# Kernel optimization log

Hardware: AMD Instinct MI355X
Metric: run time of the kernel (lower is better)

Reference implementation:

```python
import jax, jax.numpy as jnp
import numpy as np
from jax import lax

# Dims
HID = 2048          # hidden_size
DI = 4096           # d_inner = expand * hidden
NH = 64             # mamba heads
P = 64              # head dim
N = 128             # d_state
G = 1               # n_groups
K = 4               # conv kernel
IM = 8192           # MLP intermediate
BB, L = 2, 2048
EPS = 1e-5
CONV_DIM = DI + 2 * G * N            # 4352
D_IN_PROJ = 2 * DI + 2 * G * N + NH  # 8512


def rmsnorm(x, w, eps=EPS):
    v = jnp.mean(jnp.square(x), axis=-1, keepdims=True)
    return x * jax.lax.rsqrt(v + eps) * w


def setup_inputs() -> dict:
    key = jax.random.key(0)
    ks = jax.random.split(key, 16)
    s = 0.02
    return {
        "positions": jnp.broadcast_to(jnp.arange(L, dtype=jnp.int32), (BB, L)),
        "hidden_states": jax.random.normal(ks[0], (BB, L, HID), jnp.float32),
        "residual": jax.random.normal(ks[1], (BB, L, HID), jnp.float32),
        "in_proj_w": jax.random.normal(ks[2], (D_IN_PROJ, HID), jnp.float32) * s,
        "conv_w": jax.random.normal(ks[3], (CONV_DIM, K), jnp.float32) * 0.2,
        "conv_b": jax.random.normal(ks[4], (CONV_DIM,), jnp.float32) * 0.02,
        "A_log": jnp.log(jnp.arange(1, NH + 1, dtype=jnp.float32)),
        "D": jnp.ones((NH,), jnp.float32),
        "dt_bias": jax.random.uniform(ks[5], (NH,), jnp.float32, -4.0, -2.0),
        "mixer_norm_w": jnp.ones((DI,), jnp.float32),
        "out_proj_w": jax.random.normal(ks[6], (HID, DI), jnp.float32) * s,
        "input_ln_w": jnp.ones((HID,), jnp.float32),
        "pre_ff_ln_w": jnp.ones((HID,), jnp.float32),
        "gate_up_w": jax.random.normal(ks[7], (2 * IM, HID), jnp.float32) * s,
        "down_w": jax.random.normal(ks[8], (HID, IM), jnp.float32) * s,
    }


def reference(positions, hidden_states, residual, in_proj_w, conv_w, conv_b,
              A_log, D, dt_bias, mixer_norm_w, out_proj_w, input_ln_w,
              pre_ff_ln_w, gate_up_w, down_w):
    del positions  # not used by the mamba mixer math
    B_, Lq, _ = hidden_states.shape

    # --- input RMSNorm with fused residual add ---
    residual = hidden_states + residual
    hs = rmsnorm(residual, input_ln_w)

    # --- Mamba2 mixer ---
    proj = jnp.einsum('bld,ed->ble', hs, in_proj_w)   # [B,L,D_IN_PROJ]
    z = proj[..., :DI]
    xBC = proj[..., DI:DI + CONV_DIM]
    dt = proj[..., DI + CONV_DIM:]                    # [B,L,NH]

    # causal depthwise conv (kernel K) + SiLU
    xp = jnp.pad(xBC, ((0, 0), (K - 1, 0), (0, 0)))
    conv = conv_b
    for k in range(K):
        conv = conv + xp[:, k:k + Lq, :] * conv_w[:, k]
    xBC = jax.nn.silu(conv)

    x = xBC[..., :DI].reshape(B_, Lq, NH, P)
    Bm = xBC[..., DI:DI + G * N].reshape(B_, Lq, G, N)
    Cm = xBC[..., DI + G * N:].reshape(B_, Lq, G, N)
    rep = NH // G
    Bm = jnp.repeat(Bm, rep, axis=2)                  # [B,L,NH,N]
    Cm = jnp.repeat(Cm, rep, axis=2)

    dt = jax.nn.softplus(dt + dt_bias)                # [B,L,NH]
    A = -jnp.exp(A_log)                               # [NH]
    dA = jnp.exp(dt * A)                              # [B,L,NH]

    def step(h, inp):
        x_t, B_t, C_t, dA_t, dt_t = inp               # [B,NH,P],[B,NH,N],[B,NH,N],[B,NH],[B,NH]
        h = dA_t[..., None, None] * h + \
            (dt_t[..., None, None] * x_t[..., None]) * B_t[:, :, None, :]
        y = jnp.einsum('bhpn,bhn->bhp', h, C_t)
        return h, y

    xs = (x.transpose(1, 0, 2, 3), Bm.transpose(1, 0, 2, 3),
          Cm.transpose(1, 0, 2, 3), dA.transpose(1, 0, 2), dt.transpose(1, 0, 2))
    h0 = jnp.zeros((B_, NH, P, N), hidden_states.dtype)
    _, ys = lax.scan(step, h0, xs)                    # [L,B,NH,P]
    y = ys.transpose(1, 0, 2, 3) + D[None, None, :, None] * x
    y = y.reshape(B_, Lq, DI)

    # gated RMSNorm (Mixer2RMSNormGated, n_groups=1)
    y = y * jax.nn.silu(z)
    y = rmsnorm(y, mixer_norm_w)
    mamba_out = jnp.einsum('bld,hd->blh', y, out_proj_w)

    # --- pre-FF RMSNorm with fused residual add ---
    residual2 = mamba_out + residual
    hs2 = rmsnorm(residual2, pre_ff_ln_w)

    # --- gated MLP (SiluAndMul) ---
    gu = jnp.einsum('bld,ed->ble', hs2, gate_up_w)    # [B,L,2*IM]
    act = jax.nn.silu(gu[..., :IM]) * gu[..., IM:]
    out = jnp.einsum('bli,hi->blh', act, down_w)
    return out, residual2
```

## Files before the change

### kernel.cpp

```cpp
#include <hip/hip_runtime.h>

#define T_TOK 4096
#define HID   2048
#define DI    4096
#define NH    64
#define PDIM  64
#define NSTATE 128
#define IM    8192
#define LSEQ  2048
#define CONVD 4352
#define DPROJ 8512
#define DPADR 8704
#define QC    64
#define NCH   32

typedef __bf16 bf16x8 __attribute__((ext_vector_type(8)));
typedef float  f32x4  __attribute__((ext_vector_type(4)));

__device__ __forceinline__ unsigned short f2bf(float f) {
  unsigned u = __float_as_uint(f);
  u = (u + 0x7fffu + ((u >> 16) & 1u)) >> 16;
  return (unsigned short)u;
}
__device__ __forceinline__ float bf2f(unsigned short h) {
  return __uint_as_float(((unsigned)h) << 16);
}
__device__ __forceinline__ float siluf(float x) {
  return x / (1.f + __expf(-x));
}

#define GLL(gaddr, laddr) __builtin_amdgcn_global_load_lds( \
    (const __attribute__((address_space(1))) void*)(gaddr), \
    (__attribute__((address_space(3))) void*)(laddr), 16, 0, 0)

__device__ __forceinline__ void cvt8(const float* __restrict__ s, unsigned short* __restrict__ d) {
  float4 v0 = *(const float4*)s;
  float4 v1 = *(const float4*)(s + 4);
  unsigned short o[8];
  o[0] = f2bf(v0.x); o[1] = f2bf(v0.y); o[2] = f2bf(v0.z); o[3] = f2bf(v0.w);
  o[4] = f2bf(v1.x); o[5] = f2bf(v1.y); o[6] = f2bf(v1.z); o[7] = f2bf(v1.w);
  *(uint4*)d = *(const uint4*)o;
}

#define CV_IN_END  2228224ULL
#define CV_OUT_END 3276800ULL
#define CV_GU_END  7471104ULL
#define CV_DN_END  9568256ULL

__global__ __launch_bounds__(256)
void k_cvt_all(const float* __restrict__ w_in, const float* __restrict__ w_out,
               const float* __restrict__ w_gu, const float* __restrict__ w_dn,
               unsigned short* __restrict__ d_in, unsigned short* __restrict__ d_out,
               unsigned short* __restrict__ d_gu, unsigned short* __restrict__ d_dn) {
  size_t gid = (size_t)blockIdx.x * 256 + threadIdx.x;
  if (gid < CV_IN_END) {
    size_t idx8 = gid * 8;
    int r = (int)(idx8 >> 11), k = (int)(idx8 & 2047);
    if (r < DPROJ) {
      cvt8(&w_in[(size_t)r * HID + k], d_in + idx8);
    } else {
      uint4 z = {0, 0, 0, 0};
      *(uint4*)(d_in + idx8) = z;
    }
  } else if (gid < CV_OUT_END) {
    size_t idx8 = (gid - CV_IN_END) * 8;
    cvt8(w_out + idx8, d_out + idx8);
  } else if (gid < CV_GU_END) {
    size_t idx8 = (gid - CV_OUT_END) * 8;
    int r = (int)(idx8 >> 11), k = (int)(idx8 & 2047);
    int g = r >> 6, j = r & 63;
    int srcr = (j < 32) ? (g * 32 + j) : (IM + g * 32 + (j - 32));
    cvt8(&w_gu[(size_t)srcr * HID + k], d_gu + idx8);
  } else if (gid < CV_DN_END) {
    size_t idx8 = (gid - CV_GU_END) * 8;
    cvt8(w_dn + idx8, d_dn + idx8);
  }
}

template <int EPI, int BM>
__global__ __launch_bounds__(512, 2)
void gemm8(const unsigned short* __restrict__ A, const unsigned short* __restrict__ W,
           int K, int ldo, void* __restrict__ outp,
           const float* __restrict__ resid) {
  constexpr int MREP  = BM / 32;
  constexpr int ABYT  = BM * 128;
  constexpr int BUFB  = ABYT + 32768;
  constexpr int NTM   = 4096 / BM;
  __shared__ __align__(16) char smem[2 * BUFB];
  const int t = threadIdx.x;
  const int w = t >> 6, l = t & 63;
  const int lr = l & 15, hi = l >> 4;
  const int wr = w >> 2, wc = w & 3;

  const int q = (int)gridDim.x >> 3;
  const int bid = blockIdx.x;
  const int id2 = (bid & 7) * q + (bid >> 3);
  const int tn = id2 / NTM, tm = id2 % NTM;
  const int m0b = tm * BM, n0b = tn << 8;

  const int srow = t >> 3;
  const int scole = ((t & 7) << 3) ^ ((t & 32) ? 16 : 0) ^ ((t & 64) ? 32 : 0);
  const unsigned short* Ag = A + (size_t)(m0b + srow) * K + scole;
  const unsigned short* Wg = W + (size_t)(n0b + srow) * K + scole;
  const int ldsw = w * 1024;

  const int fa = ((lr & 4) ? 32 : 0) | ((lr & 8) ? 64 : 0);
  const int arow = (wr * (BM / 2) + lr) * 128 + hi * 16;
  const int brow = (wc * 64 + lr) * 128 + hi * 16;
  const int aoff0 = arow ^ fa, aoff1 = (arow + 64) ^ fa;
  const int boff0 = brow ^ fa, boff1 = (brow + 64) ^ fa;

#define ISSUE_A(jt, bb) do {                                                    \
    _Pragma("unroll")                                                           \
    for (int p_ = 0; p_ < BM / 64; ++p_)                                        \
      GLL(Ag + (size_t)(p_ * 64) * K + (size_t)(jt) * 64,                       \
          smem + (bb) * BUFB + p_ * 8192 + ldsw); } while (0)
#define ISSUE_B(jt, bb) do {                                                    \
    _Pragma("unroll")                                                           \
    for (int p_ = 0; p_ < 4; ++p_)                                              \
      GLL(Wg + (size_t)(p_ * 64) * K + (size_t)(jt) * 64,                       \
          smem + (bb) * BUFB + ABYT + p_ * 8192 + ldsw); } while (0)

#define RDF(off, base) (*(const bf16x8*)((base) + (off)))
#define MF(P, x, y, c0, c1, c2, c3) do {                                                     \
    __builtin_amdgcn_s_setprio(1);                                                           \
    acc[2*(P)  ][0] = __builtin_amdgcn_mfma_f32_16x16x32_bf16((x),(c0),acc[2*(P)  ][0],0,0,0);\
    acc[2*(P)+1][0] = __builtin_amdgcn_mfma_f32_16x16x32_bf16((y),(c0),acc[2*(P)+1][0],0,0,0);\
    acc[2*(P)  ][1] = __builtin_amdgcn_mfma_f32_16x16x32_bf16((x),(c1),acc[2*(P)  ][1],0,0,0);\
    acc[2*(P)+1][1] = __builtin_amdgcn_mfma_f32_16x16x32_bf16((y),(c1),acc[2*(P)+1][1],0,0,0);\
    acc[2*(P)  ][2] = __builtin_amdgcn_mfma_f32_16x16x32_bf16((x),(c2),acc[2*(P)  ][2],0,0,0);\
    acc[2*(P)+1][2] = __builtin_amdgcn_mfma_f32_16x16x32_bf16((y),(c2),acc[2*(P)+1][2],0,0,0);\
    acc[2*(P)  ][3] = __builtin_amdgcn_mfma_f32_16x16x32_bf16((x),(c3),acc[2*(P)  ][3],0,0,0);\
    acc[2*(P)+1][3] = __builtin_amdgcn_mfma_f32_16x16x32_bf16((y),(c3),acc[2*(P)+1][3],0,0,0);\
    __builtin_amdgcn_s_setprio(0); } while (0)

  f32x4 acc[MREP][4];
#pragma unroll
  for (int m = 0; m < MREP; m++)
#pragma unroll
    for (int n = 0; n < 4; n++) acc[m][n] = (f32x4){0.f, 0.f, 0.f, 0.f};

  const int nkt = K >> 6;
  ISSUE_A(0, 0); ISSUE_B(0, 0);

  for (int j = 0; j < nkt; ++j) {
    const int cur = j & 1;
    const char* Ab = smem + cur * BUFB;
    const char* Bb = Ab + ABYT;
    asm volatile("s_waitcnt vmcnt(0)" ::: "memory");
    __builtin_amdgcn_s_barrier();
    __builtin_amdgcn_sched_barrier(0);
    if (j + 1 < nkt) { ISSUE_A(j + 1, cur ^ 1); ISSUE_B(j + 1, cur ^ 1); }
    bf16x8 b0 = RDF(boff0, Bb), b1 = RDF(boff0 + 2048, Bb),
           b2 = RDF(boff0 + 4096, Bb), b3 = RDF(boff0 + 6144, Bb);
    bf16x8 af0 = RDF(aoff0, Ab), af1 = RDF(aoff0 + 2048, Ab);
    bf16x8 af2, af3, b4, b5, b6, b7;
    if constexpr (MREP == 8) {
      af2 = RDF(aoff0 + 4096, Ab); af3 = RDF(aoff0 + 6144, Ab);
      MF(0, af0, af1, b0, b1, b2, b3);
      af0 = RDF(aoff0 + 8192, Ab); af1 = RDF(aoff0 + 10240, Ab);
      MF(1, af2, af3, b0, b1, b2, b3);
      af2 = RDF(aoff0 + 12288, Ab); af3 = RDF(aoff0 + 14336, Ab);
      MF(2, af0, af1, b0, b1, b2, b3);
      b4 = RDF(boff1, Bb); b5 = RDF(boff1 + 2048, Bb);
      b6 = RDF(boff1 + 4096, Bb); b7 = RDF(boff1 + 6144, Bb);
      af0 = RDF(aoff1, Ab); af1 = RDF(aoff1 + 2048, Ab);
      MF(3, af2, af3, b0, b1, b2, b3);
      af2 = RDF(aoff1 + 4096, Ab); af3 = RDF(aoff1 + 6144, Ab);
      MF(0, af0, af1, b4, b5, b6, b7);
      af0 = RDF(aoff1 + 8192, Ab); af1 = RDF(aoff1 + 10240, Ab);
      MF(1, af2, af3, b4, b5, b6, b7);
      af2 = RDF(aoff1 + 12288, Ab); af3 = RDF(aoff1 + 14336, Ab);
      MF(2, af0, af1, b4, b5, b6, b7);
      MF(3, af2, af3, b4, b5, b6, b7);
    } else {
      af2 = RDF(aoff0 + 4096, Ab); af3 = RDF(aoff0 + 6144, Ab);
      MF(0, af0, af1, b0, b1, b2, b3);
      b4 = RDF(boff1, Bb); b5 = RDF(boff1 + 2048, Bb);
      b6 = RDF(boff1 + 4096, Bb); b7 = RDF(boff1 + 6144, Bb);
      af0 = RDF(aoff1, Ab); af1 = RDF(aoff1 + 2048, Ab);
      MF(1, af2, af3, b0, b1, b2, b3);
      af2 = RDF(aoff1 + 4096, Ab); af3 = RDF(aoff1 + 6144, Ab);
      MF(0, af0, af1, b4, b5, b6, b7);
      MF(1, af2, af3, b4, b5, b6, b7);
    }
  }

  if constexpr (EPI == 0) {
    unsigned short* op = (unsigned short*)outp;
#pragma unroll
    for (int m = 0; m < MREP; m++)
#pragma unroll
      for (int n = 0; n < 4; n++)
#pragma unroll
        for (int r = 0; r < 4; r++) {
          int row = m0b + wr * (BM / 2) + m * 16 + hi * 4 + r;
          int col = n0b + wc * 64 + n * 16 + lr;
          op[(size_t)row * ldo + col] = f2bf(acc[m][n][r]);
        }
  } else if constexpr (EPI == 2) {
    unsigned short* op = (unsigned short*)outp;
    const int gbase = (n0b + wc * 64) >> 1;
#pragma unroll
    for (int m = 0; m < MREP; m++)
#pragma unroll
      for (int n = 0; n < 2; n++)
#pragma unroll
        for (int r = 0; r < 4; r++) {
          int row = m0b + wr * (BM / 2) + m * 16 + hi * 4 + r;
          int col = gbase + n * 16 + lr;
          float g = acc[m][n][r], u = acc[m][n + 2][r];
          op[(size_t)row * ldo + col] = f2bf(siluf(g) * u);
        }
  } else {
    float* op = (float*)outp;
#pragma unroll
    for (int m = 0; m < MREP; m++)
#pragma unroll
      for (int n = 0; n < 4; n++)
#pragma unroll
        for (int r = 0; r < 4; r++) {
          int row = m0b + wr * (BM / 2) + m * 16 + hi * 4 + r;
          int col = n0b + wc * 64 + n * 16 + lr;
          float v = acc[m][n][r];
          if constexpr (EPI == 1) v += resid[(size_t)row * ldo + col];
          op[(size_t)row * ldo + col] = v;
        }
  }
#undef ISSUE_A
#undef ISSUE_B
#undef RDF
#undef MF
}

__device__ __forceinline__ float block_reduce_sum256(float v, float* sred) {
#pragma unroll
  for (int m = 32; m; m >>= 1) v += __shfl_xor(v, m);
  int t = threadIdx.x;
  if ((t & 63) == 0) sred[t >> 6] = v;
  __syncthreads();
  return sred[0] + sred[1] + sred[2] + sred[3];
}

__global__ __launch_bounds__(256)
void k_addnorm(const float* __restrict__ hin, const float* __restrict__ rin,
               const float* __restrict__ wln, float* __restrict__ rout,
               unsigned short* __restrict__ hbf) {
  __shared__ float sred[4];
  const int tok = blockIdx.x, t = threadIdx.x;
  const size_t base = (size_t)tok * HID + t * 8;
  float4 a0 = *(const float4*)&hin[base];
  float4 a1 = *(const float4*)&hin[base + 4];
  float4 b0 = *(const float4*)&rin[base];
  float4 b1 = *(const float4*)&rin[base + 4];
  float v[8] = {a0.x + b0.x, a0.y + b0.y, a0.z + b0.z, a0.w + b0.w,
                a1.x + b1.x, a1.y + b1.y, a1.z + b1.z, a1.w + b1.w};
  float ss = 0.f;
#pragma unroll
  for (int j = 0; j < 8; j++) ss += v[j] * v[j];
  float tot = block_reduce_sum256(ss, sred);
  float rms = rsqrtf(tot * (1.f / HID) + 1e-5f);
  *(float4*)&rout[base] = (float4){v[0], v[1], v[2], v[3]};
  *(float4*)&rout[base + 4] = (float4){v[4], v[5], v[6], v[7]};
  float4 w0 = *(const float4*)&wln[t * 8];
  float4 w1 = *(const float4*)&wln[t * 8 + 4];
  float wa[8] = {w0.x, w0.y, w0.z, w0.w, w1.x, w1.y, w1.z, w1.w};
  unsigned short o[8];
#pragma unroll
  for (int j = 0; j < 8; j++) o[j] = f2bf(v[j] * rms * wa[j]);
  *(ushort4*)&hbf[base] = *(ushort4*)&o[0];
  *(ushort4*)&hbf[base + 4] = *(ushort4*)&o[4];
}

__global__ __launch_bounds__(256)
void k_rmsnorm_bf(const float* __restrict__ src, const float* __restrict__ wln,
                  unsigned short* __restrict__ dst) {
  __shared__ float sred[4];
  const int tok = blockIdx.x, t = threadIdx.x;
  const size_t base = (size_t)tok * HID + t * 8;
  float4 a0 = *(const float4*)&src[base];
  float4 a1 = *(const float4*)&src[base + 4];
  float v[8] = {a0.x, a0.y, a0.z, a0.w, a1.x, a1.y, a1.z, a1.w};
  float ss = 0.f;
#pragma unroll
  for (int j = 0; j < 8; j++) ss += v[j] * v[j];
  float tot = block_reduce_sum256(ss, sred);
  float rms = rsqrtf(tot * (1.f / HID) + 1e-5f);
  float4 w0 = *(const float4*)&wln[t * 8];
  float4 w1 = *(const float4*)&wln[t * 8 + 4];
  float wa[8] = {w0.x, w0.y, w0.z, w0.w, w1.x, w1.y, w1.z, w1.w};
  unsigned short o[8];
#pragma unroll
  for (int j = 0; j < 8; j++) o[j] = f2bf(v[j] * rms * wa[j]);
  *(ushort4*)&dst[base] = *(ushort4*)&o[0];
  *(ushort4*)&dst[base + 4] = *(ushort4*)&o[4];
}

__global__ __launch_bounds__(256)
void k_gatenorm(const unsigned short* __restrict__ ybuf, const unsigned short* __restrict__ projbf,
                const float* __restrict__ wmix, unsigned short* __restrict__ ynorm) {
  __shared__ float sred[4];
  const int tok = blockIdx.x, t = threadIdx.x;
  const size_t yb = (size_t)tok * DI;
  const size_t pb = (size_t)tok * DPADR;
  float g[16];
  float ss = 0.f;
#pragma unroll
  for (int j = 0; j < 16; j++) {
    int idx = j * 256 + t;
    float yv = bf2f(ybuf[yb + idx]);
    float z = bf2f(projbf[pb + idx]);
    float gg = yv * siluf(z);
    g[j] = gg;
    ss += gg * gg;
  }
  float tot = block_reduce_sum256(ss, sred);
  float rms = rsqrtf(tot * (1.f / DI) + 1e-5f);
#pragma unroll
  for (int j = 0; j < 16; j++) {
    int idx = j * 256 + t;
    ynorm[yb + idx] = f2bf(g[j] * rms * wmix[idx]);
  }
}

__global__ __launch_bounds__(256)
void k_conv(const unsigned short* __restrict__ projbf, const float* __restrict__ cw,
            const float* __restrict__ cb, const float* __restrict__ dt_bias,
            unsigned short* __restrict__ xbf, unsigned short* __restrict__ bcbf,
            float* __restrict__ dtg) {
  const int c = blockIdx.x * 256 + threadIdx.x;
  const int tk = blockIdx.y;
  if (c < CONVD) {
    const int lpos = tk & (LSEQ - 1);
    float4 wv = *(const float4*)&cw[c * 4];
    float wk[4] = {wv.x, wv.y, wv.z, wv.w};
    float acc = cb[c];
#pragma unroll
    for (int k = 0; k < 4; k++) {
      int lp = lpos - 3 + k;
      if (lp >= 0) acc += bf2f(projbf[(size_t)(tk - 3 + k) * DPADR + DI + c]) * wk[k];
    }
    unsigned short r = f2bf(siluf(acc));
    if (c < DI) xbf[(size_t)tk * DI + c] = r;
    else        bcbf[(size_t)tk * 256 + (c - DI)] = r;
  } else if (c < CONVD + NH) {
    const int hh = c - CONVD;
    float x = bf2f(projbf[(size_t)tk * DPADR + DI + c]) + dt_bias[hh];
    float dt = (x > 20.f) ? x : log1pf(__expf(x));
    dtg[(size_t)tk * NH + hh] = dt;
  }
}

__global__ __launch_bounds__(256)
void k_ssd1(const unsigned short* __restrict__ xbf, const unsigned short* __restrict__ bcbf,
            const float* __restrict__ dtg, const float* __restrict__ A_log,
            const float* __restrict__ Dv, unsigned short* __restrict__ ybuf,
            unsigned short* __restrict__ Sc, float* __restrict__ dtsum) {
  __shared__ __align__(16) char smem[60928];
  unsigned short* sBs  = (unsigned short*)(smem);
  unsigned short* sCs  = (unsigned short*)(smem + 16384);
  unsigned short* sMs  = (unsigned short*)(smem + 16384);
  unsigned short* sBsT = (unsigned short*)(smem + 32768);
  unsigned short* sXsT = (unsigned short*)(smem + 51200);
  float* sdt = (float*)(smem + 60416);
  float* sdl = (float*)(smem + 60672);

  const int bi = blockIdx.x;
  const int ch = bi & 31, h = (bi >> 5) & 63, b = bi >> 11;
  const int bh = b * NH + h;
  const int tok0 = b * LSEQ + ch * QC;
  const int t = threadIdx.x;
  const int w = t >> 6, l = t & 63, lr = l & 15, hi = l >> 4;
  const float Ah = -__expf(A_log[h]);
  const float Dh = Dv[h];

  {
    const int srow = t >> 4, scol = (t & 15) * 8;
#pragma unroll
    for (int i = 0; i < 4; i++) {
      const unsigned short* gb = bcbf + (size_t)(tok0 + srow + 16 * i) * 256 + scol;
      GLL(gb, (char*)sBs + i * 4096 + w * 1024);
      GLL(gb + 128, (char*)sCs + i * 4096 + w * 1024);
    }
  }
  if (t < QC) sdt[t] = dtg[(size_t)(tok0 + t) * NH + h];
  __syncthreads();
  if (t < QC) sdl[t] = sdt[t];
  __syncthreads();
  for (int off = 1; off < QC; off <<= 1) {
    float v = 0.f;
    if (t < QC && t >= off) v = sdl[t - off];
    __syncthreads();
    if (t < QC) sdl[t] += v;
    __syncthreads();
  }

  {
    const int s = t >> 2;
    const float DlQ = sdl[QC - 1];
    const float csc = __expf(Ah * (DlQ - sdl[s])) * sdt[s];
    const int n0 = (t & 3) * 32;
#pragma unroll
    for (int j = 0; j < 32; j++) {
      float bv = bf2f(sBs[s * 128 + n0 + j]);
      sBsT[(n0 + j) * 72 + s] = f2bf(csc * bv);
    }
    const int p0 = (t & 3) * 16;
    const unsigned short* gx = xbf + (size_t)(tok0 + s) * DI + h * 64 + p0;
    union { uint4 v; unsigned short u[8]; } x0, x1;
    x0.v = *(const uint4*)gx;
    x1.v = *(const uint4*)(gx + 8);
#pragma unroll
    for (int j = 0; j < 8; j++) {
      sXsT[(p0 + j) * 72 + s] = x0.u[j];
      sXsT[(p0 + 8 + j) * 72 + s] = x1.u[j];
    }
  }
  __syncthreads();

  f32x4 accS[4];
#pragma unroll
  for (int jf = 0; jf < 4; jf++) accS[jf] = (f32x4){0.f, 0.f, 0.f, 0.f};
#pragma unroll
  for (int ks = 0; ks < 4; ks++) {
    bf16x8 a = *(const bf16x8*)&sBs[(w * 16 + lr) * 128 + ks * 32 + hi * 8];
#pragma unroll
    for (int jf = 0; jf < 4; jf++) {
      bf16x8 bbq = *(const bf16x8*)&sCs[(jf * 16 + lr) * 128 + ks * 32 + hi * 8];
      accS[jf] = __builtin_amdgcn_mfma_f32_16x16x32_bf16(a, bbq, accS[jf], 0, 0, 0);
    }
  }
  __syncthreads();

  {
    const int s0 = w * 16 + hi * 4;
#pragma unroll
    for (int jf = 0; jf < 4; jf++) {
      const int tt = jf * 16 + lr;
      const float dlt = sdl[tt];
      unsigned short mv[4];
#pragma unroll
      for (int r = 0; r < 4; r++) {
        const int ss = s0 + r;
        float val = 0.f;
        if (ss <= tt) val = accS[jf][r] * __expf(Ah * (dlt - sdl[ss])) * sdt[ss];
        mv[r] = f2bf(val);
      }
      *(ushort4*)&sMs[tt * 72 + s0] = *(ushort4*)mv;
    }
  }
  __syncthreads();

  {
    f32x4 accY[4];
#pragma unroll
    for (int jf = 0; jf < 4; jf++) accY[jf] = (f32x4){0.f, 0.f, 0.f, 0.f};
#pragma unroll
    for (int ks = 0; ks < 2; ks++) {
      bf16x8 a = *(const bf16x8*)&sMs[(w * 16 + lr) * 72 + ks * 32 + hi * 8];
#pragma unroll
      for (int jf = 0; jf < 4; jf++) {
        bf16x8 bbq = *(const bf16x8*)&sXsT[(jf * 16 + lr) * 72 + ks * 32 + hi * 8];
        accY[jf] = __builtin_amdgcn_mfma_f32_16x16x32_bf16(a, bbq, accY[jf], 0, 0, 0);
      }
    }
#pragma unroll
    for (int jf = 0; jf < 4; jf++)
#pragma unroll
      for (int r = 0; r < 4; r++) {
        const int tt = w * 16 + hi * 4 + r;
        const int pp = jf * 16 + lr;
        float xv = bf2f(sXsT[pp * 72 + tt]);
        ybuf[(size_t)(tok0 + tt) * DI + h * 64 + pp] = f2bf(accY[jf][r] + Dh * xv);
      }
  }

  {
    f32x4 accT[8];
#pragma unroll
    for (int jf = 0; jf < 8; jf++) accT[jf] = (f32x4){0.f, 0.f, 0.f, 0.f};
#pragma unroll
    for (int ks = 0; ks < 2; ks++) {
      bf16x8 a = *(const bf16x8*)&sXsT[(w * 16 + lr) * 72 + ks * 32 + hi * 8];
#pragma unroll
      for (int jf = 0; jf < 8; jf++) {
        bf16x8 bbq = *(const bf16x8*)&sBsT[(jf * 16 + lr) * 72 + ks * 32 + hi * 8];
        accT[jf] = __builtin_amdgcn_mfma_f32_16x16x32_bf16(a, bbq, accT[jf], 0, 0, 0);
      }
    }
    unsigned short* sc = Sc + ((size_t)bh * NCH + ch) * (PDIM * NSTATE);
#pragma unroll
    for (int jf = 0; jf < 8; jf++)
#pragma unroll
      for (int r = 0; r < 4; r++) {
        const int pp = w * 16 + hi * 4 + r;
        const int nn = jf * 16 + lr;
        sc[pp * NSTATE + nn] = f2bf(accT[jf][r]);
      }
  }
  if (t == 0) dtsum[bh * NCH + ch] = sdl[QC - 1];
}

__global__ __launch_bounds__(256)
void k_ssd2(const float* __restrict__ A_log, const float* __restrict__ dtsum,
            unsigned short* __restrict__ ScHt) {
  const int blk = blockIdx.x;
  const int bh = blk >> 3, pg = blk & 7;
  const int t = threadIdx.x;
  const int p = pg * 8 + (t >> 5), n0 = (t & 31) * 4;
  const int h = bh & 63;
  const float Ah = -__expf(A_log[h]);
  float H[4] = {0.f, 0.f, 0.f, 0.f};
  for (int c = 0; c < NCH; c++) {
    size_t base = (((size_t)bh * NCH + c) * PDIM + p) * NSTATE + n0;
    ushort4 sv = *(const ushort4*)&ScHt[base];
    float dec = __expf(Ah * dtsum[bh * NCH + c]);
    ushort4 hv;
    hv.x = f2bf(H[0]); hv.y = f2bf(H[1]); hv.z = f2bf(H[2]); hv.w = f2bf(H[3]);
    *(ushort4*)&ScHt[base] = hv;
    H[0] = dec * H[0] + bf2f(sv.x);
    H[1] = dec * H[1] + bf2f(sv.y);
    H[2] = dec * H[2] + bf2f(sv.z);
    H[3] = dec * H[3] + bf2f(sv.w);
  }
}

__global__ __launch_bounds__(256)
void k_ssd3(const unsigned short* __restrict__ bcbf, const unsigned short* __restrict__ Ht,
            const float* __restrict__ dtg, const float* __restrict__ A_log,
            unsigned short* __restrict__ ybuf) {
  __shared__ __align__(16) char smem[33280];
  unsigned short* sCs = (unsigned short*)(smem);
  unsigned short* sHt = (unsigned short*)(smem + 16384);
  float* sdt = (float*)(smem + 32768);
  float* sdl = (float*)(smem + 33024);

  const int bi = blockIdx.x;
  const int ch = bi & 31, h = (bi >> 5) & 63, b = bi >> 11;
  const int bh = b * NH + h;
  const int tok0 = b * LSEQ + ch * QC;
  const int t = threadIdx.x;
  const int w = t >> 6, l = t & 63, lr = l & 15, hi = l >> 4;
  const float Ah = -__expf(A_log[h]);

  {
    const int srow = t >> 4, scol = (t & 15) * 8;
    const unsigned short* gh = Ht + ((size_t)bh * NCH + ch) * (PDIM * NSTATE);
#pragma unroll
    for (int i = 0; i < 4; i++) {
      const unsigned short* gc = bcbf + (size_t)(tok0 + srow + 16 * i) * 256 + 128 + scol;
      GLL(gc, (char*)sCs + i * 4096 + w * 1024);
      GLL(gh + i * 2048 + t * 8, (char*)sHt + i * 4096 + w * 1024);
    }
  }
  if (t < QC) sdt[t] = dtg[(size_t)(tok0 + t) * NH + h];
  __syncthreads();
  if (t < QC) sdl[t] = sdt[t];
  __syncthreads();
  for (int off = 1; off < QC; off <<= 1) {
    float v = 0.f;
    if (t < QC && t >= off) v = sdl[t - off];
    __syncthreads();
    if (t < QC) sdl[t] += v;
    __syncthreads();
  }

  f32x4 acc[4];
#pragma unroll
  for (int jf = 0; jf < 4; jf++) acc[jf] = (f32x4){0.f, 0.f, 0.f, 0.f};
#pragma unroll
  for (int ks = 0; ks < 4; ks++) {
    bf16x8 a = *(const bf16x8*)&sCs[(w * 16 + lr) * 128 + ks * 32 + hi * 8];
#pragma unroll
    for (int jf = 0; jf < 4; jf++) {
      bf16x8 bbq = *(const bf16x8*)&sHt[(jf * 16 + lr) * 128 + ks * 32 + hi * 8];
      acc[jf] = __builtin_amdgcn_mfma_f32_16x16x32_bf16(a, bbq, acc[jf], 0, 0, 0);
    }
  }
#pragma unroll
  for (int jf = 0; jf < 4; jf++)
#pragma unroll
    for (int r = 0; r < 4; r++) {
      const int tt = w * 16 + hi * 4 + r;
      const int pp = jf * 16 + lr;
      const float dec = __expf(Ah * sdl[tt]);
      const size_t o = (size_t)(tok0 + tt) * DI + h * 64 + pp;
      ybuf[o] = f2bf(bf2f(ybuf[o]) + dec * acc[jf][r]);
    }
}

static const size_t OFF_WBF_IN  = 0;
static const size_t OFF_WBF_OUT = 35651584;
static const size_t OFF_WBF_GU  = 52428800;
static const size_t OFF_WBF_DN  = 119537664;
static const size_t OFF_RESID   = 153092096;
static const size_t OFF_HSBF    = 186646528;
static const size_t OFF_PROJ    = 203423744;
static const size_t OFF_XBF     = 274726912;
static const size_t OFF_BCBF    = 308281344;
static const size_t OFF_DTG     = 310378496;
static const size_t OFF_YBUF    = 311427072;
static const size_t OFF_SC      = 344981504;
static const size_t OFF_DTSUM   = 412090368;

extern "C" void kernel_launch(void* const* d_in, const int* in_sizes, int n_in,
                              void* d_out, int out_size, void* d_ws, size_t ws_size,
                              hipStream_t stream) {
  (void)in_sizes; (void)n_in; (void)out_size; (void)ws_size;
  const float* hidden   = (const float*)d_in[1];
  const float* resin    = (const float*)d_in[2];
  const float* w_inproj = (const float*)d_in[3];
  const float* conv_w   = (const float*)d_in[4];
  const float* conv_b   = (const float*)d_in[5];
  const float* A_log    = (const float*)d_in[6];
  const float* Dvec     = (const float*)d_in[7];
  const float* dt_bias  = (const float*)d_in[8];
  const float* w_mix    = (const float*)d_in[9];
  const float* w_outp   = (const float*)d_in[10];
  const float* w_ln1    = (const float*)d_in[11];
  const float* w_ln2    = (const float*)d_in[12];
  const float* w_gu     = (const float*)d_in[13];
  const float* w_dn     = (const float*)d_in[14];

  char* ws = (char*)d_ws;
  unsigned short* wbf_in  = (unsigned short*)(ws + OFF_WBF_IN);
  unsigned short* wbf_out = (unsigned short*)(ws + OFF_WBF_OUT);
  unsigned short* wbf_gu  = (unsigned short*)(ws + OFF_WBF_GU);
  unsigned short* wbf_dn  = (unsigned short*)(ws + OFF_WBF_DN);
  float*          residb  = (float*)(ws + OFF_RESID);
  unsigned short* hsbf    = (unsigned short*)(ws + OFF_HSBF);
  unsigned short* projbf  = (unsigned short*)(ws + OFF_PROJ);
  unsigned short* actbf   = (unsigned short*)(ws + OFF_PROJ);
  unsigned short* xbf     = (unsigned short*)(ws + OFF_XBF);
  unsigned short* ynormbf = (unsigned short*)(ws + OFF_XBF);
  unsigned short* bcbf    = (unsigned short*)(ws + OFF_BCBF);
  float*          dtgb    = (float*)(ws + OFF_DTG);
  unsigned short* ybuf    = (unsigned short*)(ws + OFF_YBUF);
  unsigned short* scht    = (unsigned short*)(ws + OFF_SC);
  float*          dtsumb  = (float*)(ws + OFF_DTSUM);

  float* out0 = (float*)d_out;
  float* res2 = out0 + (size_t)T_TOK * HID;

  k_cvt_all<<<37376, 256, 0, stream>>>(w_inproj, w_outp, w_gu, w_dn,
                                       wbf_in, wbf_out, wbf_gu, wbf_dn);
  k_addnorm<<<T_TOK, 256, 0, stream>>>(hidden, resin, w_ln1, residb, hsbf);
  gemm8<0, 256><<<34 * 16, 512, 0, stream>>>(hsbf, wbf_in, HID, DPADR, projbf, nullptr);
  k_conv<<<dim3(18, T_TOK), 256, 0, stream>>>(projbf, conv_w, conv_b, dt_bias, xbf, bcbf, dtgb);
  k_ssd1<<<4096, 256, 0, stream>>>(xbf, bcbf, dtgb, A_log, Dvec, ybuf, scht, dtsumb);
  k_ssd2<<<1024, 256, 0, stream>>>(A_log, dtsumb, scht);
  k_ssd3<<<4096, 256, 0, stream>>>(bcbf, scht, dtgb, A_log, ybuf);
  k_gatenorm<<<T_TOK, 256, 0, stream>>>(ybuf, projbf, w_mix, ynormbf);
  gemm8<1, 128><<<8 * 32, 512, 0, stream>>>(ynormbf, wbf_out, DI, HID, res2, residb);
  k_rmsnorm_bf<<<T_TOK, 256, 0, stream>>>(res2, w_ln2, hsbf);
  gemm8<2, 256><<<64 * 16, 512, 0, stream>>>(hsbf, wbf_gu, HID, IM, actbf, nullptr);
  gemm8<3, 128><<<8 * 32, 512, 0, stream>>>(actbf, wbf_dn, IM, HID, out0, nullptr);
}
```

Baseline: 996.4 us.

## Replace GEMM with fixed 128x256 tile, K-step 32, unswizzled LDS, 4 blocks/CU

Replaces the templated BM GEMM with a single kernel that uses a 128x256 output tile, a K step of 32 and an unswizzled 64-byte-row LDS layout. Shared memory per block drops to 48KB and the launch bound asks for 4 blocks per CU to raise occupancy. All four projection GEMMs use it, so the in_proj and gate_up GEMMs now run smaller M tiles with twice as many blocks. The cost is fewer MFMAs per barrier, more barrier round-trips, and likely LDS bank conflicts because the XOR swizzle is gone.

```diff
diff --git a/kernel.cpp b/kernel.cpp
--- a/kernel.cpp
+++ b/kernel.cpp
@@ -77,124 +77,85 @@
   }
 }
 
-template <int EPI, int BM>
-__global__ __launch_bounds__(512, 2)
-void gemm8(const unsigned short* __restrict__ A, const unsigned short* __restrict__ W,
+template <int EPI>
+__global__ __launch_bounds__(512, 4)
+void gemmk(const unsigned short* __restrict__ A, const unsigned short* __restrict__ W,
            int K, int ldo, void* __restrict__ outp,
            const float* __restrict__ resid) {
-  constexpr int MREP  = BM / 32;
-  constexpr int ABYT  = BM * 128;
-  constexpr int BUFB  = ABYT + 32768;
-  constexpr int NTM   = 4096 / BM;
+  constexpr int ABYT = 8192;
+  constexpr int BBYT = 16384;
+  constexpr int BUFB = ABYT + BBYT;
+  constexpr int NTM  = 32;
   __shared__ __align__(16) char smem[2 * BUFB];
   const int t = threadIdx.x;
   const int w = t >> 6, l = t & 63;
   const int lr = l & 15, hi = l >> 4;
   const int wr = w >> 2, wc = w & 3;
 
-  const int q = (int)gridDim.x >> 3;
+  const int q8 = (int)gridDim.x >> 3;
   const int bid = blockIdx.x;
-  const int id2 = (bid & 7) * q + (bid >> 3);
+  const int id2 = (bid & 7) * q8 + (bid >> 3);
   const int tn = id2 / NTM, tm = id2 % NTM;
-  const int m0b = tm * BM, n0b = tn << 8;
-
-  const int srow = t >> 3;
-  const int scole = ((t & 7) << 3) ^ ((t & 32) ? 16 : 0) ^ ((t & 64) ? 32 : 0);
-  const unsigned short* Ag = A + (size_t)(m0b + srow) * K + scole;
-  const unsigned short* Wg = W + (size_t)(n0b + srow) * K + scole;
-  const int ldsw = w * 1024;
-
-  const int fa = ((lr & 4) ? 32 : 0) | ((lr & 8) ? 64 : 0);
-  const int arow = (wr * (BM / 2) + lr) * 128 + hi * 16;
-  const int brow = (wc * 64 + lr) * 128 + hi * 16;
-  const int aoff0 = arow ^ fa, aoff1 = (arow + 64) ^ fa;
-  const int boff0 = brow ^ fa, boff1 = (brow + 64) ^ fa;
-
-#define ISSUE_A(jt, bb) do {                                                    \
-    _Pragma("unroll")                                                           \
-    for (int p_ = 0; p_ < BM / 64; ++p_)                                        \
-      GLL(Ag + (size_t)(p_ * 64) * K + (size_t)(jt) * 64,                       \
-          smem + (bb) * BUFB + p_ * 8192 + ldsw); } while (0)
+  const int m0b = tm << 7, n0b = tn << 8;
+
+  const unsigned short* Ag = A + (size_t)(m0b + (t >> 2)) * K + (t & 3) * 8;
+  const unsigned short* Wg = W + (size_t)(n0b + (t >> 2)) * K + (t & 3) * 8;
+
+  const int aoffc = (wr * 64 + lr) * 64 + hi * 16;
+  const int boffc = ABYT + (wc * 64 + lr) * 64 + hi * 16;
+
+#define ISSUE_A(jt, bb) GLL(Ag + (size_t)(jt) * 32, smem + (bb) * BUFB + t * 16)
 #define ISSUE_B(jt, bb) do {                                                    \
-    _Pragma("unroll")                                                           \
-    for (int p_ = 0; p_ < 4; ++p_)                                              \
-      GLL(Wg + (size_t)(p_ * 64) * K + (size_t)(jt) * 64,                       \
-          smem + (bb) * BUFB + ABYT + p_ * 8192 + ldsw); } while (0)
+    GLL(Wg + (size_t)(jt) * 32, smem + (bb) * BUFB + ABYT + t * 16);            \
+    GLL(Wg + (size_t)128 * K + (size_t)(jt) * 32,                               \
+        smem + (bb) * BUFB + ABYT + 8192 + t * 16); } while (0)
 
 #define RDF(off, base) (*(const bf16x8*)((base) + (off)))
-#define MF(P, x, y, c0, c1, c2, c3) do {                                                     \
-    __builtin_amdgcn_s_setprio(1);                                                           \
-    acc[2*(P)  ][0] = __builtin_amdgcn_mfma_f32_16x16x32_bf16((x),(c0),acc[2*(P)  ][0],0,0,0);\
-    acc[2*(P)+1][0] = __builtin_amdgcn_mfma_f32_16x16x32_bf16((y),(c0),acc[2*(P)+1][0],0,0,0);\
-    acc[2*(P)  ][1] = __builtin_amdgcn_mfma_f32_16x16x32_bf16((x),(c1),acc[2*(P)  ][1],0,0,0);\
-    acc[2*(P)+1][1] = __builtin_amdgcn_mfma_f32_16x16x32_bf16((y),(c1),acc[2*(P)+1][1],0,0,0);\
-    acc[2*(P)  ][2] = __builtin_amdgcn_mfma_f32_16x16x32_bf16((x),(c2),acc[2*(P)  ][2],0,0,0);\
-    acc[2*(P)+1][2] = __builtin_amdgcn_mfma_f32_16x16x32_bf16((y),(c2),acc[2*(P)+1][2],0,0,0);\
-    acc[2*(P)  ][3] = __builtin_amdgcn_mfma_f32_16x16x32_bf16((x),(c3),acc[2*(P)  ][3],0,0,0);\
-    acc[2*(P)+1][3] = __builtin_amdgcn_mfma_f32_16x16x32_bf16((y),(c3),acc[2*(P)+1][3],0,0,0);\
+#define MF2(P, x, y) do {                                                                     \
+    __builtin_amdgcn_s_setprio(1);                                                            \
+    acc[2*(P)  ][0] = __builtin_amdgcn_mfma_f32_16x16x32_bf16((x), b0, acc[2*(P)  ][0],0,0,0);\
+    acc[2*(P)+1][0] = __builtin_amdgcn_mfma_f32_16x16x32_bf16((y), b0, acc[2*(P)+1][0],0,0,0);\
+    acc[2*(P)  ][1] = __builtin_amdgcn_mfma_f32_16x16x32_bf16((x), b1, acc[2*(P)  ][1],0,0,0);\
+    acc[2*(P)+1][1] = __builtin_amdgcn_mfma_f32_16x16x32_bf16((y), b1, acc[2*(P)+1][1],0,0,0);\
+    acc[2*(P)  ][2] = __builtin_amdgcn_mfma_f32_16x16x32_bf16((x), b2, acc[2*(P)  ][2],0,0,0);\
+    acc[2*(P)+1][2] = __builtin_amdgcn_mfma_f32_16x16x32_bf16((y), b2, acc[2*(P)+1][2],0,0,0);\
+    acc[2*(P)  ][3] = __builtin_amdgcn_mfma_f32_16x16x32_bf16((x), b3, acc[2*(P)  ][3],0,0,0);\
+    acc[2*(P)+1][3] = __builtin_amdgcn_mfma_f32_16x16x32_bf16((y), b3, acc[2*(P)+1][3],0,0,0);\
     __builtin_amdgcn_s_setprio(0); } while (0)
 
-  f32x4 acc[MREP][4];
-#pragma unroll
-  for (int m = 0; m < MREP; m++)
+  f32x4 acc[4][4];
+#pragma unroll
+  for (int m = 0; m < 4; m++)
 #pragma unroll
     for (int n = 0; n < 4; n++) acc[m][n] = (f32x4){0.f, 0.f, 0.f, 0.f};
 
-  const int nkt = K >> 6;
+  const int nkt = K >> 5;
   ISSUE_A(0, 0); ISSUE_B(0, 0);
 
   for (int j = 0; j < nkt; ++j) {
-    const int cur = j & 1;
-    const char* Ab = smem + cur * BUFB;
-    const char* Bb = Ab + ABYT;
+    const char* Ab = smem + (size_t)(j & 1) * BUFB;
+    const int nb = (j & 1) ^ 1;
     asm volatile("s_waitcnt vmcnt(0)" ::: "memory");
     __builtin_amdgcn_s_barrier();
     __builtin_amdgcn_sched_barrier(0);
-    if (j + 1 < nkt) { ISSUE_A(j + 1, cur ^ 1); ISSUE_B(j + 1, cur ^ 1); }
-    bf16x8 b0 = RDF(boff0, Bb), b1 = RDF(boff0 + 2048, Bb),
-           b2 = RDF(boff0 + 4096, Bb), b3 = RDF(boff0 + 6144, Bb);
-    bf16x8 af0 = RDF(aoff0, Ab), af1 = RDF(aoff0 + 2048, Ab);
-    bf16x8 af2, af3, b4, b5, b6, b7;
-    if constexpr (MREP == 8) {
-      af2 = RDF(aoff0 + 4096, Ab); af3 = RDF(aoff0 + 6144, Ab);
-      MF(0, af0, af1, b0, b1, b2, b3);
-      af0 = RDF(aoff0 + 8192, Ab); af1 = RDF(aoff0 + 10240, Ab);
-      MF(1, af2, af3, b0, b1, b2, b3);
-      af2 = RDF(aoff0 + 12288, Ab); af3 = RDF(aoff0 + 14336, Ab);
-      MF(2, af0, af1, b0, b1, b2, b3);
-      b4 = RDF(boff1, Bb); b5 = RDF(boff1 + 2048, Bb);
-      b6 = RDF(boff1 + 4096, Bb); b7 = RDF(boff1 + 6144, Bb);
-      af0 = RDF(aoff1, Ab); af1 = RDF(aoff1 + 2048, Ab);
-      MF(3, af2, af3, b0, b1, b2, b3);
-      af2 = RDF(aoff1 + 4096, Ab); af3 = RDF(aoff1 + 6144, Ab);
-      MF(0, af0, af1, b4, b5, b6, b7);
-      af0 = RDF(aoff1 + 8192, Ab); af1 = RDF(aoff1 + 10240, Ab);
-      MF(1, af2, af3, b4, b5, b6, b7);
-      af2 = RDF(aoff1 + 12288, Ab); af3 = RDF(aoff1 + 14336, Ab);
-      MF(2, af0, af1, b4, b5, b6, b7);
-      MF(3, af2, af3, b4, b5, b6, b7);
-    } else {
-      af2 = RDF(aoff0 + 4096, Ab); af3 = RDF(aoff0 + 6144, Ab);
-      MF(0, af0, af1, b0, b1, b2, b3);
-      b4 = RDF(boff1, Bb); b5 = RDF(boff1 + 2048, Bb);
-      b6 = RDF(boff1 + 4096, Bb); b7 = RDF(boff1 + 6144, Bb);
-      af0 = RDF(aoff1, Ab); af1 = RDF(aoff1 + 2048, Ab);
-      MF(1, af2, af3, b0, b1, b2, b3);
-      af2 = RDF(aoff1 + 4096, Ab); af3 = RDF(aoff1 + 6144, Ab);
-      MF(0, af0, af1, b4, b5, b6, b7);
-      MF(1, af2, af3, b4, b5, b6, b7);
-    }
+    if (j + 1 < nkt) { ISSUE_A(j + 1, nb); ISSUE_B(j + 1, nb); }
+    bf16x8 b0 = RDF(boffc, Ab), b1 = RDF(boffc + 1024, Ab),
+           b2 = RDF(boffc + 2048, Ab), b3 = RDF(boffc + 3072, Ab);
+    bf16x8 a0 = RDF(aoffc, Ab), a1 = RDF(aoffc + 1024, Ab);
+    MF2(0, a0, a1);
+    bf16x8 a2 = RDF(aoffc + 2048, Ab), a3 = RDF(aoffc + 3072, Ab);
+    MF2(1, a2, a3);
   }
 
   if constexpr (EPI == 0) {
     unsigned short* op = (unsigned short*)outp;
 #pragma unroll
-    for (int m = 0; m < MREP; m++)
+    for (int m = 0; m < 4; m++)
 #pragma unroll
       for (int n = 0; n < 4; n++)
 #pragma unroll
         for (int r = 0; r < 4; r++) {
-          int row = m0b + wr * (BM / 2) + m * 16 + hi * 4 + r;
+          int row = m0b + wr * 64 + m * 16 + hi * 4 + r;
           int col = n0b + wc * 64 + n * 16 + lr;
           op[(size_t)row * ldo + col] = f2bf(acc[m][n][r]);
         }
@@ -202,12 +163,12 @@
     unsigned short* op = (unsigned short*)outp;
     const int gbase = (n0b + wc * 64) >> 1;
 #pragma unroll
-    for (int m = 0; m < MREP; m++)
+    for (int m = 0; m < 4; m++)
 #pragma unroll
       for (int n = 0; n < 2; n++)
 #pragma unroll
         for (int r = 0; r < 4; r++) {
-          int row = m0b + wr * (BM / 2) + m * 16 + hi * 4 + r;
+          int row = m0b + wr * 64 + m * 16 + hi * 4 + r;
           int col = gbase + n * 16 + lr;
           float g = acc[m][n][r], u = acc[m][n + 2][r];
           op[(size_t)row * ldo + col] = f2bf(siluf(g) * u);
@@ -215,12 +176,12 @@
   } else {
     float* op = (float*)outp;
 #pragma unroll
-    for (int m = 0; m < MREP; m++)
+    for (int m = 0; m < 4; m++)
 #pragma unroll
       for (int n = 0; n < 4; n++)
 #pragma unroll
         for (int r = 0; r < 4; r++) {
-          int row = m0b + wr * (BM / 2) + m * 16 + hi * 4 + r;
+          int row = m0b + wr * 64 + m * 16 + hi * 4 + r;
           int col = n0b + wc * 64 + n * 16 + lr;
           float v = acc[m][n][r];
           if constexpr (EPI == 1) v += resid[(size_t)row * ldo + col];
@@ -230,7 +191,7 @@
 #undef ISSUE_A
 #undef ISSUE_B
 #undef RDF
-#undef MF
+#undef MF2
 }
 
 __device__ __forceinline__ float block_reduce_sum256(float v, float* sred) {
@@ -645,14 +606,14 @@
   k_cvt_all<<<37376, 256, 0, stream>>>(w_inproj, w_outp, w_gu, w_dn,
                                        wbf_in, wbf_out, wbf_gu, wbf_dn);
   k_addnorm<<<T_TOK, 256, 0, stream>>>(hidden, resin, w_ln1, residb, hsbf);
-  gemm8<0, 256><<<34 * 16, 512, 0, stream>>>(hsbf, wbf_in, HID, DPADR, projbf, nullptr);
+  gemmk<0><<<34 * 32, 512, 0, stream>>>(hsbf, wbf_in, HID, DPADR, projbf, nullptr);
   k_conv<<<dim3(18, T_TOK), 256, 0, stream>>>(projbf, conv_w, conv_b, dt_bias, xbf, bcbf, dtgb);
   k_ssd1<<<4096, 256, 0, stream>>>(xbf, bcbf, dtgb, A_log, Dvec, ybuf, scht, dtsumb);
   k_ssd2<<<1024, 256, 0, stream>>>(A_log, dtsumb, scht);
   k_ssd3<<<4096, 256, 0, stream>>>(bcbf, scht, dtgb, A_log, ybuf);
   k_gatenorm<<<T_TOK, 256, 0, stream>>>(ybuf, projbf, w_mix, ynormbf);
-  gemm8<1, 128><<<8 * 32, 512, 0, stream>>>(ynormbf, wbf_out, DI, HID, res2, residb);
+  gemmk<1><<<8 * 32, 512, 0, stream>>>(ynormbf, wbf_out, DI, HID, res2, residb);
   k_rmsnorm_bf<<<T_TOK, 256, 0, stream>>>(res2, w_ln2, hsbf);
-  gemm8<2, 256><<<64 * 16, 512, 0, stream>>>(hsbf, wbf_gu, HID, IM, actbf, nullptr);
-  gemm8<3, 128><<<8 * 32, 512, 0, stream>>>(actbf, wbf_dn, IM, HID, out0, nullptr);
-}
+  gemmk<2><<<64 * 32, 512, 0, stream>>>(hsbf, wbf_gu, HID, IM, actbf, nullptr);
+  gemmk<3><<<8 * 32, 512, 0, stream>>>(actbf, wbf_dn, IM, HID, out0, nullptr);
+}
```

New measurement: 1.123 ms. 1.13x slower.

## Add ping-pong pipelined 256x256 GEMM kernel for in_proj and gate_up

Applied to the files above, without the earlier changes.

Introduces gemm8p, a 256x256-tile GEMM with one block per CU that splits each K-tile's global-to-LDS staging into quarter chunks interleaved with the MFMA phases. It uses per-quarter barriers, s_setprio around the MFMA bursts and partial vmcnt waits so loads overlap compute better than the old double-buffered loop. The in_proj and gate_up GEMMs now use it, and the old gemm8 is trimmed to the BM=128 path. The trade-off is 128KB of LDS per block and occupancy of one block per CU, plus more barriers per tile.

```diff
diff --git a/kernel.cpp b/kernel.cpp
--- a/kernel.cpp
+++ b/kernel.cpp
@@ -77,6 +77,153 @@
   }
 }
 
+template <int EPI>
+__global__ __launch_bounds__(512, 1)
+void gemm8p(const unsigned short* __restrict__ A, const unsigned short* __restrict__ W,
+            int K, int ldo, void* __restrict__ outp) {
+  __shared__ __align__(16) char smem[131072];
+  const int t = threadIdx.x;
+  const int w = t >> 6, l = t & 63;
+  const int lr = l & 15, hi = l >> 4;
+  const int wr = w >> 2, wc = w & 3;
+
+  const int q8 = (int)gridDim.x >> 3;
+  const int bid = blockIdx.x;
+  const int id2 = (bid & 7) * q8 + (bid >> 3);
+  const int tn = id2 >> 4, tm = id2 & 15;
+  const int m0b = tm << 8, n0b = tn << 8;
+
+  const int srow = t >> 3;
+  const int scole = ((t & 7) << 3) ^ ((t & 32) ? 16 : 0) ^ ((t & 64) ? 32 : 0);
+  const unsigned short* Ag = A + (size_t)(m0b + srow) * K + scole;
+  const unsigned short* Wg = W + (size_t)(n0b + srow) * K + scole;
+  const int ldsw = w * 1024;
+
+  const int fa = ((lr & 4) ? 32 : 0) | ((lr & 8) ? 64 : 0);
+  const int arow = (wr * 128 + lr) * 128 + hi * 16;
+  const int brow = (wc * 64 + lr) * 128 + hi * 16;
+  const int aoff0 = arow ^ fa, aoff1 = (arow + 64) ^ fa;
+  const int boff0 = brow ^ fa, boff1 = (brow + 64) ^ fa;
+
+#define STAGE_A(jt, h, bb) do {                                                 \
+    _Pragma("unroll")                                                           \
+    for (int p_ = 0; p_ < 2; ++p_)                                              \
+      GLL(Ag + (size_t)((h) * 128 + p_ * 64) * K + (size_t)(jt) * 64,           \
+          smem + (bb) * 65536 + ((h) * 2 + p_) * 8192 + ldsw); } while (0)
+#define STAGE_B(jt, h, bb) do {                                                 \
+    _Pragma("unroll")                                                           \
+    for (int p_ = 0; p_ < 2; ++p_)                                              \
+      GLL(Wg + (size_t)((h) * 128 + p_ * 64) * K + (size_t)(jt) * 64,           \
+          smem + (bb) * 65536 + 32768 + ((h) * 2 + p_) * 8192 + ldsw); } while (0)
+
+#define RDF(off, base) (*(const bf16x8*)((base) + (off)))
+
+  f32x4 acc[8][4];
+#pragma unroll
+  for (int m = 0; m < 8; m++)
+#pragma unroll
+    for (int n = 0; n < 4; n++) acc[m][n] = (f32x4){0.f, 0.f, 0.f, 0.f};
+
+  const int nkt = K >> 6;
+  const int niter = nkt >> 1;
+
+  STAGE_A(0, 0, 0); STAGE_A(0, 1, 0);
+  STAGE_B(0, 0, 0); STAGE_B(0, 1, 0);
+  STAGE_B(1, 0, 1); STAGE_B(1, 1, 1);
+  asm volatile("s_waitcnt vmcnt(4)" ::: "memory");
+  __builtin_amdgcn_s_barrier();
+  __builtin_amdgcn_sched_barrier(0);
+
+  for (int it = 0; it < niter; ++it) {
+    const int T0 = 2 * it;
+#pragma unroll
+    for (int g = 0; g < 2; ++g) {
+      const char* Ab = smem + g * 65536;
+      const char* Bb = Ab + 32768;
+      bf16x8 bfr[8];
+#pragma unroll
+      for (int q = 0; q < 4; ++q) {
+        if (q == 0) {
+#pragma unroll
+          for (int n = 0; n < 4; n++) {
+            bfr[n]     = RDF(boff0 + n * 2048, Bb);
+            bfr[4 + n] = RDF(boff1 + n * 2048, Bb);
+          }
+        }
+        bf16x8 a0 = RDF(aoff0 + (2 * q) * 2048, Ab);
+        bf16x8 a1 = RDF(aoff0 + (2 * q + 1) * 2048, Ab);
+        bf16x8 a2 = RDF(aoff1 + (2 * q) * 2048, Ab);
+        bf16x8 a3 = RDF(aoff1 + (2 * q + 1) * 2048, Ab);
+        if (g == 0) {
+          if (q == 0)      STAGE_A(T0 + 1, 0, 1);
+          else if (q == 1) STAGE_A(T0 + 1, 1, 1);
+          else if (q == 2) { if (T0 + 2 < nkt) STAGE_B(T0 + 2, 0, 0); }
+          else             { if (T0 + 2 < nkt) STAGE_B(T0 + 2, 1, 0); }
+        } else {
+          if (q == 0)      { if (T0 + 2 < nkt) STAGE_A(T0 + 2, 0, 0); }
+          else if (q == 1) { if (T0 + 2 < nkt) STAGE_A(T0 + 2, 1, 0); }
+          else if (q == 2) { if (T0 + 3 < nkt) STAGE_B(T0 + 3, 0, 1); }
+          else             { if (T0 + 3 < nkt) STAGE_B(T0 + 3, 1, 1); }
+        }
+        __builtin_amdgcn_sched_barrier(0);
+        __builtin_amdgcn_s_barrier();
+        __builtin_amdgcn_sched_barrier(0);
+        __builtin_amdgcn_s_setprio(1);
+#pragma unroll
+        for (int n = 0; n < 4; n++) {
+          acc[2 * q][n]     = __builtin_amdgcn_mfma_f32_16x16x32_bf16(a0, bfr[n], acc[2 * q][n], 0, 0, 0);
+          acc[2 * q + 1][n] = __builtin_amdgcn_mfma_f32_16x16x32_bf16(a1, bfr[n], acc[2 * q + 1][n], 0, 0, 0);
+        }
+#pragma unroll
+        for (int n = 0; n < 4; n++) {
+          acc[2 * q][n]     = __builtin_amdgcn_mfma_f32_16x16x32_bf16(a2, bfr[4 + n], acc[2 * q][n], 0, 0, 0);
+          acc[2 * q + 1][n] = __builtin_amdgcn_mfma_f32_16x16x32_bf16(a3, bfr[4 + n], acc[2 * q + 1][n], 0, 0, 0);
+        }
+        __builtin_amdgcn_s_setprio(0);
+        __builtin_amdgcn_sched_barrier(0);
+        if (q == 3) {
+          const int lastStaged = (g == 0) ? (T0 + 2) : (T0 + 3);
+          if (lastStaged < nkt) asm volatile("s_waitcnt vmcnt(4)" ::: "memory");
+          else                  asm volatile("s_waitcnt vmcnt(0)" ::: "memory");
+        }
+        __builtin_amdgcn_s_barrier();
+        __builtin_amdgcn_sched_barrier(0);
+      }
+    }
+  }
+
+  if constexpr (EPI == 0) {
+    unsigned short* op = (unsigned short*)outp;
+#pragma unroll
+    for (int m = 0; m < 8; m++)
+#pragma unroll
+      for (int n = 0; n < 4; n++)
+#pragma unroll
+        for (int r = 0; r < 4; r++) {
+          int row = m0b + wr * 128 + m * 16 + hi * 4 + r;
+          int col = n0b + wc * 64 + n * 16 + lr;
+          op[(size_t)row * ldo + col] = f2bf(acc[m][n][r]);
+        }
+  } else {
+    unsigned short* op = (unsigned short*)outp;
+    const int gbase = (n0b + wc * 64) >> 1;
+#pragma unroll
+    for (int m = 0; m < 8; m++)
+#pragma unroll
+      for (int n = 0; n < 2; n++)
+#pragma unroll
+        for (int r = 0; r < 4; r++) {
+          int row = m0b + wr * 128 + m * 16 + hi * 4 + r;
+          int col = gbase + n * 16 + lr;
+          float gg = acc[m][n][r], u = acc[m][n + 2][r];
+          op[(size_t)row * ldo + col] = f2bf(siluf(gg) * u);
+        }
+  }
+#undef STAGE_A
+#undef STAGE_B
+#undef RDF
+}
+
 template <int EPI, int BM>
 __global__ __launch_bounds__(512, 2)
 void gemm8(const unsigned short* __restrict__ A, const unsigned short* __restrict__ W,
@@ -155,78 +302,32 @@
            b2 = RDF(boff0 + 4096, Bb), b3 = RDF(boff0 + 6144, Bb);
     bf16x8 af0 = RDF(aoff0, Ab), af1 = RDF(aoff0 + 2048, Ab);
     bf16x8 af2, af3, b4, b5, b6, b7;
-    if constexpr (MREP == 8) {
-      af2 = RDF(aoff0 + 4096, Ab); af3 = RDF(aoff0 + 6144, Ab);
-      MF(0, af0, af1, b0, b1, b2, b3);
-      af0 = RDF(aoff0 + 8192, Ab); af1 = RDF(aoff0 + 10240, Ab);
-      MF(1, af2, af3, b0, b1, b2, b3);
-      af2 = RDF(aoff0 + 12288, Ab); af3 = RDF(aoff0 + 14336, Ab);
-      MF(2, af0, af1, b0, b1, b2, b3);
-      b4 = RDF(boff1, Bb); b5 = RDF(boff1 + 2048, Bb);
-      b6 = RDF(boff1 + 4096, Bb); b7 = RDF(boff1 + 6144, Bb);
-      af0 = RDF(aoff1, Ab); af1 = RDF(aoff1 + 2048, Ab);
-      MF(3, af2, af3, b0, b1, b2, b3);
-      af2 = RDF(aoff1 + 4096, Ab); af3 = RDF(aoff1 + 6144, Ab);
-      MF(0, af0, af1, b4, b5, b6, b7);
-      af0 = RDF(aoff1 + 8192, Ab); af1 = RDF(aoff1 + 10240, Ab);
-      MF(1, af2, af3, b4, b5, b6, b7);
-      af2 = RDF(aoff1 + 12288, Ab); af3 = RDF(aoff1 + 14336, Ab);
-      MF(2, af0, af1, b4, b5, b6, b7);
-      MF(3, af2, af3, b4, b5, b6, b7);
-    } else {
-      af2 = RDF(aoff0 + 4096, Ab); af3 = RDF(aoff0 + 6144, Ab);
-      MF(0, af0, af1, b0, b1, b2, b3);
-      b4 = RDF(boff1, Bb); b5 = RDF(boff1 + 2048, Bb);
-      b6 = RDF(boff1 + 4096, Bb); b7 = RDF(boff1 + 6144, Bb);
-      af0 = RDF(aoff1, Ab); af1 = RDF(aoff1 + 2048, Ab);
-      MF(1, af2, af3, b0, b1, b2, b3);
-      af2 = RDF(aoff1 + 4096, Ab); af3 = RDF(aoff1 + 6144, Ab);
-      MF(0, af0, af1, b4, b5, b6, b7);
-      MF(1, af2, af3, b4, b5, b6, b7);
-    }
-  }
-
-  if constexpr (EPI == 0) {
-    unsigned short* op = (unsigned short*)outp;
-#pragma unroll
-    for (int m = 0; m < MREP; m++)
-#pragma unroll
-      for (int n = 0; n < 4; n++)
-#pragma unroll
-        for (int r = 0; r < 4; r++) {
-          int row = m0b + wr * (BM / 2) + m * 16 + hi * 4 + r;
-          int col = n0b + wc * 64 + n * 16 + lr;
-          op[(size_t)row * ldo + col] = f2bf(acc[m][n][r]);
+    af2 = RDF(aoff0 + 4096, Ab); af3 = RDF(aoff0 + 6144, Ab);
+    MF(0, af0, af1, b0, b1, b2, b3);
+    b4 = RDF(boff1, Bb); b5 = RDF(boff1 + 2048, Bb);
+    b6 = RDF(boff1 + 4096, Bb); b7 = RDF(boff1 + 6144, Bb);
+    af0 = RDF(aoff1, Ab); af1 = RDF(aoff1 + 2048, Ab);
+    MF(1, af2, af3, b0, b1, b2, b3);
+    af2 = RDF(aoff1 + 4096, Ab); af3 = RDF(aoff1 + 6144, Ab);
+    MF(0, af0, af1, b4, b5, b6, b7);
+    MF(1, af2, af3, b4, b5, b6, b7);
+  }
+
+#pragma unroll
+  for (int m = 0; m < MREP; m++)
+#pragma unroll
+    for (int n = 0; n < 4; n++)
+#pragma unroll
+      for (int r = 0; r < 4; r++) {
+        int row = m0b + wr * (BM / 2) + m * 16 + hi * 4 + r;
+        int col = n0b + wc * 64 + n * 16 + lr;
+        float v = acc[m][n][r];
+        if constexpr (EPI == 1) {
+          ((float*)outp)[(size_t)row * ldo + col] = v + resid[(size_t)row * ldo + col];
+        } else {
+          ((float*)outp)[(size_t)row * ldo + col] = v;
         }
-  } else if constexpr (EPI == 2) {
-    unsigned short* op = (unsigned short*)outp;
-    const int gbase = (n0b + wc * 64) >> 1;
-#pragma unroll
-    for (int m = 0; m < MREP; m++)
-#pragma unroll
-      for (int n = 0; n < 2; n++)
-#pragma unroll
-        for (int r = 0; r < 4; r++) {
-          int row = m0b + wr * (BM / 2) + m * 16 + hi * 4 + r;
-          int col = gbase + n * 16 + lr;
-          float g = acc[m][n][r], u = acc[m][n + 2][r];
-          op[(size_t)row * ldo + col] = f2bf(siluf(g) * u);
-        }
-  } else {
-    float* op = (float*)outp;
-#pragma unroll
-    for (int m = 0; m < MREP; m++)
-#pragma unroll
-      for (int n = 0; n < 4; n++)
-#pragma unroll
-        for (int r = 0; r < 4; r++) {
-          int row = m0b + wr * (BM / 2) + m * 16 + hi * 4 + r;
-          int col = n0b + wc * 64 + n * 16 + lr;
-          float v = acc[m][n][r];
-          if constexpr (EPI == 1) v += resid[(size_t)row * ldo + col];
-          op[(size_t)row * ldo + col] = v;
-        }
-  }
+      }
 #undef ISSUE_A
 #undef ISSUE_B
 #undef RDF
@@ -645,7 +746,7 @@
   k_cvt_all<<<37376, 256, 0, stream>>>(w_inproj, w_outp, w_gu, w_dn,
                                        wbf_in, wbf_out, wbf_gu, wbf_dn);
   k_addnorm<<<T_TOK, 256, 0, stream>>>(hidden, resin, w_ln1, residb, hsbf);
-  gemm8<0, 256><<<34 * 16, 512, 0, stream>>>(hsbf, wbf_in, HID, DPADR, projbf, nullptr);
+  gemm8p<0><<<34 * 16, 512, 0, stream>>>(hsbf, wbf_in, HID, DPADR, projbf);
   k_conv<<<dim3(18, T_TOK), 256, 0, stream>>>(projbf, conv_w, conv_b, dt_bias, xbf, bcbf, dtgb);
   k_ssd1<<<4096, 256, 0, stream>>>(xbf, bcbf, dtgb, A_log, Dvec, ybuf, scht, dtsumb);
   k_ssd2<<<1024, 256, 0, stream>>>(A_log, dtsumb, scht);
@@ -653,6 +754,6 @@
   k_gatenorm<<<T_TOK, 256, 0, stream>>>(ybuf, projbf, w_mix, ynormbf);
   gemm8<1, 128><<<8 * 32, 512, 0, stream>>>(ynormbf, wbf_out, DI, HID, res2, residb);
   k_rmsnorm_bf<<<T_TOK, 256, 0, stream>>>(res2, w_ln2, hsbf);
-  gemm8<2, 256><<<64 * 16, 512, 0, stream>>>(hsbf, wbf_gu, HID, IM, actbf, nullptr);
+  gemm8p<2><<<64 * 16, 512, 0, stream>>>(hsbf, wbf_gu, HID, IM, actbf);
   gemm8<3, 128><<<8 * 32, 512, 0, stream>>>(actbf, wbf_dn, IM, HID, out0, nullptr);
 }
```

New measurement: 1.027 ms. 1.03x slower.
